# Kernel tuning notes

Measured on AMD Instinct MI355X. Metric: run time of the kernel, lower is better.

The kernel has to match this reference:

```python
import jax, jax.numpy as jnp
import numpy as np

M = 2048      # mention groups (spans with antecedents)
K_MAX = 128   # max antecedents per mention
N = 4096      # candidate span pool
G = 1000      # span representation dim
D = 20        # distance/genre/speaker embed dim
H = 150       # Score MLP hidden
GIJ = 3 * G + 3 * D  # 3060


def setup_inputs() -> dict:
    key = jax.random.key(0)
    ks = jax.random.split(key, 12)
    # ragged group lengths (deterministic): cycle 1..K_MAX, sum = P = 132096
    lengths = np.tile(np.arange(1, K_MAX + 1), M // K_MAX).astype(np.int32)
    P = int(lengths.sum())
    seg_ids = np.repeat(np.arange(M), lengths).astype(np.int32)
    starts = np.cumsum(lengths) - lengths
    offsets = (np.arange(P) - starts[seg_ids]).astype(np.int32)

    genre_emb = jax.random.normal(ks[3], (8, D), jnp.float32) * 0.02
    genre_emb = genre_emb.at[0].set(0.0)   # padding_idx=0
    speaker_emb = jax.random.normal(ks[4], (3, D), jnp.float32) * 0.02
    speaker_emb = speaker_emb.at[0].set(0.0)  # padding_idx=0

    return {
        "g_i": jax.random.normal(ks[0], (N, G), jnp.float32),
        "mention_scores": jax.random.normal(ks[1], (N, 1), jnp.float32),
        "dist_emb": jax.random.normal(ks[2], (9, D), jnp.float32) * 0.02,
        "genre_emb": genre_emb,
        "speaker_emb": speaker_emb,
        "W1": jax.random.normal(ks[5], (GIJ, H), jnp.float32) / np.sqrt(GIJ),
        "b1": jnp.zeros((H,), jnp.float32),
        "W2": jax.random.normal(ks[6], (H, H), jnp.float32) / np.sqrt(H),
        "b2": jnp.zeros((H,), jnp.float32),
        "W3": jax.random.normal(ks[7], (H, 1), jnp.float32) / np.sqrt(H),
        "b3": jnp.zeros((1,), jnp.float32),
        "mention_ids": jax.random.randint(ks[8], (P,), 0, N, jnp.int32),
        "antecedent_ids": jax.random.randint(ks[9], (P,), 0, N, jnp.int32),
        "dist_ids": jax.random.randint(ks[10], (P,), 0, 9, jnp.int32),
        "genre_ids": jax.random.randint(ks[11], (P,), 0, 8, jnp.int32),
        "speaker_ids": jax.random.randint(jax.random.fold_in(key, 99), (P,), 0, 3, jnp.int32),
        "lengths": jnp.asarray(lengths),
        "seg_ids": jnp.asarray(seg_ids),
        "offsets": jnp.asarray(offsets),
    }


def reference(g_i, mention_scores, dist_emb, genre_emb, speaker_emb,
              W1, b1, W2, b2, W3, b3,
              mention_ids, antecedent_ids, dist_ids, genre_ids, speaker_ids,
              lengths, seg_ids, offsets):
    # feature gathers: phi = [distance, genre, speaker] embeddings, (P, 3D)
    phi = jnp.concatenate(
        [dist_emb[dist_ids], genre_emb[genre_ids], speaker_emb[speaker_ids]], axis=1)
    i_g = g_i[mention_ids]      # (P, G)
    j_g = g_i[antecedent_ids]   # (P, G)
    pairs = jnp.concatenate([i_g, j_g, i_g * j_g, phi], axis=1)  # (P, GIJ)

    # 3-layer scoring MLP (dropout inactive at eval)
    h = jax.nn.relu(pairs @ W1 + b1)
    h = jax.nn.relu(h @ W2 + b2)
    s_ij = (h @ W3 + b3)[:, 0]  # (P,)

    scores = mention_scores[mention_ids, 0] + mention_scores[antecedent_ids, 0] + s_ij

    # per-group softmax over [group scores, epsilon=0] via segment ops
    seg_max = jax.ops.segment_max(scores, seg_ids, num_segments=M)
    m = jnp.maximum(seg_max, 0.0)                      # include epsilon 0
    e = jnp.exp(scores - m[seg_ids])                   # (P,)
    eps_e = jnp.exp(-m)                                # (M,)
    denom = jax.ops.segment_sum(e, seg_ids, num_segments=M) + eps_e
    pair_probs = e / denom[seg_ids]                    # (P,)
    eps_probs = eps_e / denom                          # (M,)

    # pad_and_stack(value=1000): row 0 is the empty leading group -> [1, 1000...]
    grid = jnp.full((M + 1, K_MAX + 1), 1000.0, dtype=scores.dtype)
    grid = grid.at[seg_ids + 1, offsets].set(pair_probs)
    grid = grid.at[jnp.arange(M) + 1, lengths].set(eps_probs)
    grid = grid.at[0, 0].set(1.0)
    return grid
```

## Files before the change

kernel.cpp:

```cpp
#include <hip/hip_runtime.h>

#define P_TOTAL 132096
#define NPOOL   4096
#define GDIM    1000
#define HDIM    150
#define MGRP    2048
#define KMAX    128

typedef __attribute__((ext_vector_type(4))) float f32x4;
typedef __attribute__((ext_vector_type(2))) float f32x2;
typedef __attribute__((ext_vector_type(4))) unsigned int u32x4;

#define OFF_W1C8   0
#define OFF_W1AB8  163840
#define OFF_W2F8   491520
#define OFF_ABPRE  517120
#define OFF_TABS2  3138560
#define OFF_SGRID  3276800
#define OFF_GF8    4325376
#define OFF_ITAB   8519680

__device__ __forceinline__ short f2bf(float f) {
  union { float f; unsigned u; } v; v.f = f;
  unsigned r = v.u + 0x7FFFu + ((v.u >> 16) & 1u);
  return (short)(r >> 16);
}
__device__ __forceinline__ float bf2f(unsigned short s) {
  return __builtin_bit_cast(float, ((unsigned)s) << 16);
}
__device__ __forceinline__ unsigned char f2fp8(float f) {
  int d = __builtin_amdgcn_cvt_pk_fp8_f32(f, 0.f, 0, false);
  return (unsigned char)(d & 0xFF);
}
__device__ __forceinline__ long mk64(unsigned lo, unsigned hi) {
  return (long)(((unsigned long long)hi << 32) | lo);
}

__device__ __forceinline__ u32x4 fp8prod16(u32x4 m, u32x4 a) {
  u32x4 r;
  #pragma unroll
  for (int d = 0; d < 4; ++d) {
    f32x2 ml = __builtin_amdgcn_cvt_pk_f32_fp8(m[d], false);
    f32x2 mh = __builtin_amdgcn_cvt_pk_f32_fp8(m[d], true);
    f32x2 al = __builtin_amdgcn_cvt_pk_f32_fp8(a[d], false);
    f32x2 ah = __builtin_amdgcn_cvt_pk_f32_fp8(a[d], true);
    f32x2 pl = ml * al, ph = mh * ah;
    int o = __builtin_amdgcn_cvt_pk_fp8_f32(pl[0], pl[1], 0, false);
    o = __builtin_amdgcn_cvt_pk_fp8_f32(ph[0], ph[1], o, true);
    r[d] = (unsigned)o;
  }
  return r;
}

__device__ __forceinline__ unsigned pk_bf16(float lo, float hi) {
  unsigned o;
  asm("v_cvt_pk_bf16_f32 %0, %1, %2" : "=v"(o) : "v"(lo), "v"(hi));
  return o;
}

#define S1 5120
#define S2 10240
#define S3 800
#define S4 (NPOOL*256)
#define S5 (216*160)
#define S6 P_TOTAL
__global__ __launch_bounds__(256) void prep_kernel(
    const float* __restrict__ W1, const float* __restrict__ W2,
    const float* __restrict__ g_i,
    const float* __restrict__ dist_emb, const float* __restrict__ genre_emb,
    const float* __restrict__ spk_emb, const float* __restrict__ b1,
    const int* __restrict__ did, const int* __restrict__ gid,
    const int* __restrict__ sid,
    unsigned char* __restrict__ w1c8, unsigned char* __restrict__ w1ab8,
    unsigned char* __restrict__ w2f8, unsigned* __restrict__ gf8,
    float* __restrict__ tabs2, unsigned char* __restrict__ itab8) {
  int idx = blockIdx.x * 256 + threadIdx.x;
  if (idx < S1) {
    int c = idx / 160, n = idx % 160;
    int s = c >> 1, j = c & 1;
    unsigned dw[8];
    #pragma unroll
    for (int d = 0; d < 8; ++d) {
      unsigned acc = 0;
      #pragma unroll
      for (int b = 0; b < 4; ++b) {
        int kk = d*4 + b;
        int g = kk >> 3, i = kk & 7;
        int q = g ^ ((n >> 2) & 3);
        int k = s*64 + q*16 + j*8 + i;
        float v = (k < GDIM && n < HDIM) ? W1[(2000 + k)*HDIM + n] : 0.f;
        acc |= ((unsigned)f2fp8(v)) << (8*b);
      }
      dw[d] = acc;
    }
    u32x4 lo = {dw[0], dw[1], dw[2], dw[3]};
    u32x4 hi = {dw[4], dw[5], dw[6], dw[7]};
    *(u32x4*)(w1c8 + c*5120 + n*32)      = lo;
    *(u32x4*)(w1c8 + c*5120 + n*32 + 16) = hi;
  } else if (idx < S1 + S2) {
    int i2 = idx - S1;
    int c = i2 / 320, n = i2 % 320;
    int s = c >> 2, j = c & 3;
    unsigned dw[8];
    #pragma unroll
    for (int d = 0; d < 8; ++d) {
      unsigned acc = 0;
      #pragma unroll
      for (int b = 0; b < 4; ++b) {
        int kk = d*4 + b;
        int g = kk >> 3, i = kk & 7;
        int k = s*128 + g*32 + j*8 + i;
        float v = 0.f;
        if (k < GDIM) {
          if (n < HDIM)                 v = W1[k*HDIM + n];
          else if (n >= 160 && n < 310) v = W1[(1000 + k)*HDIM + (n - 160)];
        }
        acc |= ((unsigned)f2fp8(v)) << (8*b);
      }
      dw[d] = acc;
    }
    u32x4 lo = {dw[0], dw[1], dw[2], dw[3]};
    u32x4 hi = {dw[4], dw[5], dw[6], dw[7]};
    *(u32x4*)(w1ab8 + c*10240 + n*32)      = lo;
    *(u32x4*)(w1ab8 + c*10240 + n*32 + 16) = hi;
  } else if (idx < S1 + S2 + S3) {
    int i2 = idx - S1 - S2;
    int c = i2 / 160, n = i2 % 160;
    unsigned dw[8];
    #pragma unroll
    for (int d = 0; d < 8; ++d) {
      unsigned acc = 0;
      #pragma unroll
      for (int b = 0; b < 4; ++b) {
        int kk = d*4 + b;
        int g = kk >> 3, ii = kk & 7;
        int q = g ^ ((n >> 2) & 3);
        int k = c*32 + q*8 + ii;
        float v = (k < HDIM && n < HDIM) ? W2[k*HDIM + n] : 0.f;
        acc |= ((unsigned)f2fp8(v)) << (8*b);
      }
      dw[d] = acc;
    }
    u32x4 lo = {dw[0], dw[1], dw[2], dw[3]};
    u32x4 hi = {dw[4], dw[5], dw[6], dw[7]};
    *(u32x4*)(w2f8 + c*5120 + n*32)      = lo;
    *(u32x4*)(w2f8 + c*5120 + n*32 + 16) = hi;
  } else if (idx < S1 + S2 + S3 + S4) {
    int i = idx - S1 - S2 - S3;
    int row = i >> 8, jd = i & 255;
    int c0 = jd * 4;
    float f0 = (c0     < GDIM) ? g_i[row*GDIM + c0]     : 0.f;
    float f1 = (c0 + 1 < GDIM) ? g_i[row*GDIM + c0 + 1] : 0.f;
    float f2 = (c0 + 2 < GDIM) ? g_i[row*GDIM + c0 + 2] : 0.f;
    float f3 = (c0 + 3 < GDIM) ? g_i[row*GDIM + c0 + 3] : 0.f;
    int d = 0;
    d = __builtin_amdgcn_cvt_pk_fp8_f32(f0, f1, d, false);
    d = __builtin_amdgcn_cvt_pk_fp8_f32(f2, f3, d, true);
    gf8[i] = (unsigned)d;
  } else if (idx < S1 + S2 + S3 + S4 + S5) {
    int i = idx - S1 - S2 - S3 - S4;
    int row = i / 160, n = i % 160;
    float acc = 0.f;
    if (n < HDIM) {
      int d = row / 24, g = (row / 3) % 8, sp = row % 3;
      acc = b1[n];
      #pragma unroll
      for (int kk = 0; kk < 20; ++kk) {
        acc += dist_emb [d*20 + kk]  * W1[(3000 + kk)*HDIM + n];
        acc += genre_emb[g*20 + kk]  * W1[(3020 + kk)*HDIM + n];
        acc += spk_emb  [sp*20 + kk] * W1[(3040 + kk)*HDIM + n];
      }
    }
    tabs2[i] = acc;
  } else if (idx < S1 + S2 + S3 + S4 + S5 + S6) {
    int p = idx - (S1 + S2 + S3 + S4 + S5);
    itab8[p] = (unsigned char)(did[p]*24 + gid[p]*3 + sid[p]);
  }
}

__global__ __launch_bounds__(256) void pre_gemm_kernel(
    const unsigned char* __restrict__ gf8, const unsigned char* __restrict__ w1ab8,
    unsigned short* __restrict__ abpre) {
  int wave = threadIdx.x >> 6, lane = threadIdx.x & 63;
  int quad = lane >> 4, n16 = lane & 15;
  int row0 = blockIdx.x * 64 + wave * 16;
  int col0 = blockIdx.y * 16;

  f32x4 acc = (f32x4){0.f, 0.f, 0.f, 0.f};
  const unsigned char* arow  = gf8 + (long)(row0 + n16) * 1024 + quad*32;
  const unsigned char* bbase = w1ab8 + ((long)col0 + n16) * 32 + quad*8;

  #pragma unroll 4
  for (int c = 0; c < 32; ++c) {
    long a = *(const long*)(arow + (c >> 2)*128 + (c & 3)*8);
    long b = *(const long*)(bbase + (long)c * 10240);
    acc = __builtin_amdgcn_mfma_f32_16x16x32_fp8_fp8(a, b, acc, 0, 0, 0);
  }
  #pragma unroll
  for (int r = 0; r < 4; ++r)
    abpre[(long)(row0 + quad*4 + r) * 320 + col0 + n16] = (unsigned short)f2bf(acc[r]);
}

__global__ __launch_bounds__(256) void mlp_kernel(
    const unsigned char* __restrict__ gf8,
    const unsigned* __restrict__ abpre32,
    const float* __restrict__ tabs2,
    const unsigned char* __restrict__ itab8,
    const unsigned char* __restrict__ w1c8,
    const unsigned char* __restrict__ w2f8,
    const float* __restrict__ ms,
    const float* __restrict__ W3, const float* __restrict__ b2,
    const float* __restrict__ b3,
    const int* __restrict__ mention_ids, const int* __restrict__ antecedent_ids,
    const int* __restrict__ seg_ids, const int* __restrict__ offs,
    float* __restrict__ sgrid) {

  __shared__ __align__(16) unsigned char lds[53248];

  int tid = threadIdx.x;
  int wave = tid >> 6, lane = tid & 63;
  int quad = lane >> 4, n16 = lane & 15;
  int lp0 = blockIdx.x * 128;
  int gp0 = lp0;
  int wrow = wave * 32;

  int jj = (lane & 3) ^ ((lane >> 2) & 3) ^ ((lane >> 4) & 1);
  int srow = lane >> 2;
  int swA = quad ^ (n16 & 3) ^ ((n16 >> 2) & 1);
  int swB = quad ^ ((n16 >> 2) & 3);

  const unsigned char* pA0 =
      gf8 + (long)mention_ids[gp0 + wave*16 + srow] * 1024 + jj*16;
  const unsigned char* pA1 =
      gf8 + (long)mention_ids[gp0 + (wave + 4)*16 + srow] * 1024 + jj*16;
  const unsigned char* pA2 =
      gf8 + (long)antecedent_ids[gp0 + wave*16 + srow] * 1024 + jj*16;
  const unsigned char* pA3 =
      gf8 + (long)antecedent_ids[gp0 + (wave + 4)*16 + srow] * 1024 + jj*16;
  int dA0 = wave*1024,      dA1 = (wave + 4)*1024;
  int dA2 = 8192 + dA0,     dA3 = 8192 + dA1;

  f32x4 acc0[10], acc1[10];
  #pragma unroll
  for (int t = 0; t < 10; ++t) {
    acc0[t] = (f32x4){0.f, 0.f, 0.f, 0.f};
    acc1[t] = (f32x4){0.f, 0.f, 0.f, 0.f};
  }

  auto issue = [&](int s, int buf) {
    unsigned char* base = lds + buf*26624;
    long so = (long)s * 64;
    __builtin_amdgcn_global_load_lds((const unsigned int*)(pA0 + so),
        (unsigned int*)(base + dA0 + lane*16), 16, 0, 0);
    __builtin_amdgcn_global_load_lds((const unsigned int*)(pA1 + so),
        (unsigned int*)(base + dA1 + lane*16), 16, 0, 0);
    __builtin_amdgcn_global_load_lds((const unsigned int*)(pA2 + so),
        (unsigned int*)(base + dA2 + lane*16), 16, 0, 0);
    __builtin_amdgcn_global_load_lds((const unsigned int*)(pA3 + so),
        (unsigned int*)(base + dA3 + lane*16), 16, 0, 0);
    const unsigned char* wsrc = w1c8 + (long)s*10240;
    __builtin_amdgcn_global_load_lds((const unsigned int*)(wsrc + wave*1024 + (long)lane*16),
        (unsigned int*)(base + 16384 + wave*1024 + lane*16), 16, 0, 0);
    __builtin_amdgcn_global_load_lds((const unsigned int*)(wsrc + (wave+4)*1024 + (long)lane*16),
        (unsigned int*)(base + 16384 + (wave+4)*1024 + lane*16), 16, 0, 0);
    if (wave < 2)
      __builtin_amdgcn_global_load_lds((const unsigned int*)(wsrc + (wave+8)*1024 + (long)lane*16),
          (unsigned int*)(base + 16384 + (wave+8)*1024 + lane*16), 16, 0, 0);
  };

  issue(0, 0);
  for (int s = 0; s < 16; ++s) {
    __syncthreads();
    if (s < 15) issue(s + 1, (s + 1) & 1);
    const unsigned char* cb = lds + (s & 1)*26624;

    u32x4 M0 = *(const u32x4*)(cb + (wrow + n16)*64 + swA*16);
    u32x4 C0 = *(const u32x4*)(cb + 8192 + (wrow + n16)*64 + swA*16);
    u32x4 M1 = *(const u32x4*)(cb + (wrow + 16 + n16)*64 + swA*16);
    u32x4 C1 = *(const u32x4*)(cb + 8192 + (wrow + 16 + n16)*64 + swA*16);
    u32x4 P0 = fp8prod16(M0, C0);
    u32x4 P1 = fp8prod16(M1, C1);

    #pragma unroll
    for (int j = 0; j < 2; ++j) {
      long a0 = (j == 0) ? mk64(P0[0], P0[1]) : mk64(P0[2], P0[3]);
      long a1 = (j == 0) ? mk64(P1[0], P1[1]) : mk64(P1[2], P1[3]);
      const unsigned char* bp = cb + 16384 + j*5120 + n16*32 + swB*8;
      #pragma unroll
      for (int t = 0; t < 10; ++t) {
        long b = *(const long*)(bp + t*512);
        acc0[t] = __builtin_amdgcn_mfma_f32_16x16x32_fp8_fp8(a0, b, acc0[t], 0, 0, 0);
        acc1[t] = __builtin_amdgcn_mfma_f32_16x16x32_fp8_fp8(a1, b, acc1[t], 0, 0, 0);
      }
    }
  }
  __syncthreads();

  unsigned* extw = (unsigned*)(lds + 23552 + wave*5376);
  const unsigned short* ext16 = (const unsigned short*)extw;
  unsigned char* h1w = lds + wave * 5888;
  int rowi = lane >> 2, q4 = lane & 3;

  #pragma unroll
  for (int p = 0; p < 2; ++p) {
    int gpe = gp0 + wrow + p*16 + rowi;
    int m  = mention_ids[gpe];
    int a  = antecedent_ids[gpe];
    int it = itab8[gpe];
    const u32x4* pm = (const u32x4*)(abpre32 + (long)m*160 + q4*20);
    const u32x4* pa = (const u32x4*)(abpre32 + (long)a*160 + 80 + q4*20);
    const f32x4* tb = (const f32x4*)(tabs2 + (long)it*160 + q4*40);
    #pragma unroll
    for (int k = 0; k < 5; ++k) {
      u32x4 um = pm[k], ua = pa[k];
      f32x4 ta = tb[2*k], tc = tb[2*k + 1];
      u32x4 ov;
      #pragma unroll
      for (int d = 0; d < 4; ++d) {
        float f0 = (d == 0) ? ta[0] : (d == 1) ? ta[2] : (d == 2) ? tc[0] : tc[2];
        float f1 = (d == 0) ? ta[1] : (d == 1) ? ta[3] : (d == 2) ? tc[1] : tc[3];
        float v0 = bf2f((unsigned short)(um[d] & 0xffff))
                 + bf2f((unsigned short)(ua[d] & 0xffff)) + f0;
        float v1 = bf2f((unsigned short)(um[d] >> 16))
                 + bf2f((unsigned short)(ua[d] >> 16)) + f1;
        ov[d] = pk_bf16(v0, v1);
      }
      *(u32x4*)(extw + rowi*84 + q4*20 + 4*k) = ov;
    }
    #pragma unroll
    for (int r = 0; r < 4; ++r) {
      int lr = quad*4 + r;
      #pragma unroll
      for (int t = 0; t < 10; ++t) {
        int n = t*16 + n16;
        float e = bf2f(ext16[lr*168 + n]);
        float v = ((p == 0) ? acc0[t][r] : acc1[t][r]) + e;
        h1w[(p*16 + lr)*184 + n] = f2fp8(fmaxf(v, 0.f));
      }
    }
    __syncthreads();
  }

  for (int r = wave; r < 25; r += 4) {
    __builtin_amdgcn_global_load_lds(
        (const unsigned int*)(w2f8 + r*1024 + (long)lane*16),
        (unsigned int*)(lds + 23552 + r*1024), 16, 0, 0);
  }

  float bias3 = b3[0];
  float w3v[10], b2v[10];
  #pragma unroll
  for (int t = 0; t < 10; ++t) {
    int n = t*16 + n16;
    w3v[t] = (n < HDIM) ? W3[n] : 0.f;
    b2v[t] = (n < HDIM) ? b2[n] : 0.f;
  }
  __syncthreads();

  #pragma unroll
  for (int tile = 0; tile < 2; ++tile) {
    f32x4 acc2[10];
    #pragma unroll
    for (int t = 0; t < 10; ++t) acc2[t] = (f32x4){0.f, 0.f, 0.f, 0.f};

    #pragma unroll
    for (int c = 0; c < 5; ++c) {
      long a = *(const long*)(h1w + (tile*16 + n16)*184 + c*32 + quad*8);
      const unsigned char* bp = lds + 23552 + (c*160 + n16)*32 + swB*8;
      #pragma unroll
      for (int t = 0; t < 10; ++t) {
        long b = *(const long*)(bp + t*512);
        acc2[t] = __builtin_amdgcn_mfma_f32_16x16x32_fp8_fp8(a, b, acc2[t], 0, 0, 0);
      }
    }

    float part[4] = {0.f, 0.f, 0.f, 0.f};
    #pragma unroll
    for (int t = 0; t < 10; ++t) {
      #pragma unroll
      for (int r = 0; r < 4; ++r) {
        float h2 = fmaxf(acc2[t][r] + b2v[t], 0.f);
        part[r] += h2 * w3v[t];
      }
    }
    for (int msk = 1; msk < 16; msk <<= 1) {
      #pragma unroll
      for (int r = 0; r < 4; ++r) part[r] += __shfl_xor(part[r], msk);
    }

    if (n16 == 0) {
      #pragma unroll
      for (int r = 0; r < 4; ++r) {
        int gp = gp0 + wrow + tile*16 + quad*4 + r;
        float sc = part[r] + bias3 + ms[mention_ids[gp]] + ms[antecedent_ids[gp]];
        sgrid[seg_ids[gp] * KMAX + offs[gp]] = sc;
      }
    }
  }
}

__global__ __launch_bounds__(128) void softmax_kernel(const float* __restrict__ sgrid,
                                                      const int* __restrict__ lengths,
                                                      float* __restrict__ out) {
  int b = blockIdx.x, t = threadIdx.x;
  if (b == 0) {
    out[t] = (t == 0) ? 1.0f : 1000.0f;
    if (t == 0) out[128] = 1000.0f;
    return;
  }
  int m = b - 1;
  int len = lengths[m];
  float s = (t < len) ? sgrid[m * KMAX + t] : -1e30f;

  __shared__ float redA[2];
  __shared__ float redB[2];

  float v = s;
  #pragma unroll
  for (int o = 32; o >= 1; o >>= 1) v = fmaxf(v, __shfl_xor(v, o));
  if ((t & 63) == 0) redA[t >> 6] = v;
  __syncthreads();
  float mx = fmaxf(fmaxf(redA[0], redA[1]), 0.0f);

  float e = (t < len) ? expf(s - mx) : 0.f;
  float sum = e;
  #pragma unroll
  for (int o = 32; o >= 1; o >>= 1) sum += __shfl_xor(sum, o);
  if ((t & 63) == 0) redB[t >> 6] = sum;
  __syncthreads();

  float eps_e = expf(-mx);
  float denom = redB[0] + redB[1] + eps_e;

  float* row = out + (long)(m + 1) * 129;
  float val;
  if (t < len)       val = e / denom;
  else if (t == len) val = eps_e / denom;
  else               val = 1000.0f;
  row[t] = val;
  if (t == 0) row[128] = (len == KMAX) ? (eps_e / denom) : 1000.0f;
}

extern "C" void kernel_launch(void* const* d_in, const int* in_sizes, int n_in,
                              void* d_out, int out_size, void* d_ws, size_t ws_size,
                              hipStream_t stream) {
  const float* g_i        = (const float*)d_in[0];
  const float* ms         = (const float*)d_in[1];
  const float* dist_emb   = (const float*)d_in[2];
  const float* genre_emb  = (const float*)d_in[3];
  const float* spk_emb    = (const float*)d_in[4];
  const float* W1         = (const float*)d_in[5];
  const float* b1         = (const float*)d_in[6];
  const float* W2         = (const float*)d_in[7];
  const float* b2         = (const float*)d_in[8];
  const float* W3         = (const float*)d_in[9];
  const float* b3         = (const float*)d_in[10];
  const int* mention_ids    = (const int*)d_in[11];
  const int* antecedent_ids = (const int*)d_in[12];
  const int* dist_ids       = (const int*)d_in[13];
  const int* genre_ids      = (const int*)d_in[14];
  const int* spk_ids        = (const int*)d_in[15];
  const int* lengths        = (const int*)d_in[16];
  const int* seg_ids        = (const int*)d_in[17];
  const int* offsets        = (const int*)d_in[18];

  char* ws = (char*)d_ws;
  unsigned char* w1c8  = (unsigned char*)(ws + OFF_W1C8);
  unsigned char* w1ab8 = (unsigned char*)(ws + OFF_W1AB8);
  unsigned char* w2f8  = (unsigned char*)(ws + OFF_W2F8);
  unsigned short* abpre = (unsigned short*)(ws + OFF_ABPRE);
  float* tabs2  = (float*)(ws + OFF_TABS2);
  float* sgrid  = (float*)(ws + OFF_SGRID);
  unsigned char* gf8  = (unsigned char*)(ws + OFF_GF8);
  unsigned char* itab8 = (unsigned char*)(ws + OFF_ITAB);

  const int prepN = S1 + S2 + S3 + S4 + S5 + S6;
  prep_kernel<<<(prepN + 255)/256, 256, 0, stream>>>(W1, W2, g_i,
                                                     dist_emb, genre_emb, spk_emb, b1,
                                                     dist_ids, genre_ids, spk_ids,
                                                     w1c8, w1ab8, w2f8,
                                                     (unsigned*)gf8, tabs2, itab8);
  dim3 gpre(NPOOL/64, 20);
  pre_gemm_kernel<<<gpre, 256, 0, stream>>>(gf8, w1ab8, abpre);
  mlp_kernel<<<P_TOTAL/128, 256, 0, stream>>>(gf8, (const unsigned*)abpre, tabs2, itab8,
                                              w1c8, w2f8, ms,
                                              W3, b2, b3,
                                              mention_ids, antecedent_ids,
                                              seg_ids, offsets, sgrid);
  softmax_kernel<<<MGRP + 1, 128, 0, stream>>>(sgrid, lengths, (float*)d_out);
}
```

Before: 214.2 us.

## Read MLP weights directly from global memory to shrink LDS and raise occupancy

The main MLP kernel no longer stages W1 and W2 tiles in shared memory. Each wave reads those weight fragments straight from global memory, which lets the LDS footprint drop from 52KB to 40KB and adds a launch-bounds hint for four blocks per CU. The h1 buffer gets an XOR swizzle in place of padding, and one barrier plus the W2 staging step are removed. The pre-GEMM kernel is restructured so each wave computes five 16-column tiles and reuses its A fragments across them. The risk is that direct global weight loads are less coalesced and rely on cache hits, which could expose latency in the MFMA loop.

```diff
diff --git a/kernel.cpp b/kernel.cpp
--- a/kernel.cpp
+++ b/kernel.cpp
@@ -178,30 +178,46 @@
   }
 }
 
-__global__ __launch_bounds__(256) void pre_gemm_kernel(
+__global__ __launch_bounds__(128) void pre_gemm_kernel(
     const unsigned char* __restrict__ gf8, const unsigned char* __restrict__ w1ab8,
     unsigned short* __restrict__ abpre) {
   int wave = threadIdx.x >> 6, lane = threadIdx.x & 63;
   int quad = lane >> 4, n16 = lane & 15;
-  int row0 = blockIdx.x * 64 + wave * 16;
-  int col0 = blockIdx.y * 16;
-
-  f32x4 acc = (f32x4){0.f, 0.f, 0.f, 0.f};
-  const unsigned char* arow  = gf8 + (long)(row0 + n16) * 1024 + quad*32;
-  const unsigned char* bbase = w1ab8 + ((long)col0 + n16) * 32 + quad*8;
-
-  #pragma unroll 4
-  for (int c = 0; c < 32; ++c) {
-    long a = *(const long*)(arow + (c >> 2)*128 + (c & 3)*8);
-    long b = *(const long*)(bbase + (long)c * 10240);
-    acc = __builtin_amdgcn_mfma_f32_16x16x32_fp8_fp8(a, b, acc, 0, 0, 0);
-  }
-  #pragma unroll
-  for (int r = 0; r < 4; ++r)
-    abpre[(long)(row0 + quad*4 + r) * 320 + col0 + n16] = (unsigned short)f2bf(acc[r]);
-}
-
-__global__ __launch_bounds__(256) void mlp_kernel(
+  int rowbase = blockIdx.x * 32 + wave * 16;
+  int colbase = blockIdx.y * 80;
+
+  f32x4 acc[5];
+  #pragma unroll
+  for (int t = 0; t < 5; ++t) acc[t] = (f32x4){0.f, 0.f, 0.f, 0.f};
+
+  const unsigned char* arow = gf8 + (long)(rowbase + n16) * 1024 + quad*32;
+
+  for (int s = 0; s < 8; ++s) {
+    u32x4 Aa = *(const u32x4*)(arow + s*128);
+    u32x4 Ab = *(const u32x4*)(arow + s*128 + 16);
+    #pragma unroll
+    for (int j = 0; j < 4; ++j) {
+      long a = (j == 0) ? mk64(Aa[0], Aa[1]) : (j == 1) ? mk64(Aa[2], Aa[3])
+             : (j == 2) ? mk64(Ab[0], Ab[1]) : mk64(Ab[2], Ab[3]);
+      const unsigned char* bp = w1ab8 + (((s*4 + j)*320 + colbase + n16) * 32 + quad*8);
+      #pragma unroll
+      for (int t = 0; t < 5; ++t) {
+        long b = *(const long*)(bp + t*16*32);
+        acc[t] = __builtin_amdgcn_mfma_f32_16x16x32_fp8_fp8(a, b, acc[t], 0, 0, 0);
+      }
+    }
+  }
+  #pragma unroll
+  for (int t = 0; t < 5; ++t) {
+    #pragma unroll
+    for (int r = 0; r < 4; ++r) {
+      int row = rowbase + quad*4 + r;
+      abpre[(long)row * 320 + colbase + t*16 + n16] = (unsigned short)f2bf(acc[t][r]);
+    }
+  }
+}
+
+__global__ __launch_bounds__(256, 4) void mlp_kernel(
     const unsigned char* __restrict__ gf8,
     const unsigned* __restrict__ abpre32,
     const float* __restrict__ tabs2,
@@ -215,7 +231,7 @@
     const int* __restrict__ seg_ids, const int* __restrict__ offs,
     float* __restrict__ sgrid) {
 
-  __shared__ __align__(16) unsigned char lds[53248];
+  __shared__ __align__(16) unsigned char lds[40960];
 
   int tid = threadIdx.x;
   int wave = tid >> 6, lane = tid & 63;
@@ -248,7 +264,7 @@
   }
 
   auto issue = [&](int s, int buf) {
-    unsigned char* base = lds + buf*26624;
+    unsigned char* base = lds + buf*16384;
     long so = (long)s * 64;
     __builtin_amdgcn_global_load_lds((const unsigned int*)(pA0 + so),
         (unsigned int*)(base + dA0 + lane*16), 16, 0, 0);
@@ -258,21 +274,13 @@
         (unsigned int*)(base + dA2 + lane*16), 16, 0, 0);
     __builtin_amdgcn_global_load_lds((const unsigned int*)(pA3 + so),
         (unsigned int*)(base + dA3 + lane*16), 16, 0, 0);
-    const unsigned char* wsrc = w1c8 + (long)s*10240;
-    __builtin_amdgcn_global_load_lds((const unsigned int*)(wsrc + wave*1024 + (long)lane*16),
-        (unsigned int*)(base + 16384 + wave*1024 + lane*16), 16, 0, 0);
-    __builtin_amdgcn_global_load_lds((const unsigned int*)(wsrc + (wave+4)*1024 + (long)lane*16),
-        (unsigned int*)(base + 16384 + (wave+4)*1024 + lane*16), 16, 0, 0);
-    if (wave < 2)
-      __builtin_amdgcn_global_load_lds((const unsigned int*)(wsrc + (wave+8)*1024 + (long)lane*16),
-          (unsigned int*)(base + 16384 + (wave+8)*1024 + lane*16), 16, 0, 0);
   };
 
   issue(0, 0);
   for (int s = 0; s < 16; ++s) {
     __syncthreads();
     if (s < 15) issue(s + 1, (s + 1) & 1);
-    const unsigned char* cb = lds + (s & 1)*26624;
+    const unsigned char* cb = lds + (s & 1)*16384;
 
     u32x4 M0 = *(const u32x4*)(cb + (wrow + n16)*64 + swA*16);
     u32x4 C0 = *(const u32x4*)(cb + 8192 + (wrow + n16)*64 + swA*16);
@@ -281,11 +289,12 @@
     u32x4 P0 = fp8prod16(M0, C0);
     u32x4 P1 = fp8prod16(M1, C1);
 
+    const unsigned char* wbase = w1c8 + (long)s*10240;
     #pragma unroll
     for (int j = 0; j < 2; ++j) {
       long a0 = (j == 0) ? mk64(P0[0], P0[1]) : mk64(P0[2], P0[3]);
       long a1 = (j == 0) ? mk64(P1[0], P1[1]) : mk64(P1[2], P1[3]);
-      const unsigned char* bp = cb + 16384 + j*5120 + n16*32 + swB*8;
+      const unsigned char* bp = wbase + j*5120 + n16*32 + swB*8;
       #pragma unroll
       for (int t = 0; t < 10; ++t) {
         long b = *(const long*)(bp + t*512);
@@ -296,9 +305,9 @@
   }
   __syncthreads();
 
-  unsigned* extw = (unsigned*)(lds + 23552 + wave*5376);
+  unsigned char* h1w = lds + wave * 5120;
+  unsigned* extw = (unsigned*)(lds + 20480 + wave*5120);
   const unsigned short* ext16 = (const unsigned short*)extw;
-  unsigned char* h1w = lds + wave * 5888;
   int rowi = lane >> 2, q4 = lane & 3;
 
   #pragma unroll
@@ -325,26 +334,21 @@
                  + bf2f((unsigned short)(ua[d] >> 16)) + f1;
         ov[d] = pk_bf16(v0, v1);
       }
-      *(u32x4*)(extw + rowi*84 + q4*20 + 4*k) = ov;
+      *(u32x4*)(extw + rowi*80 + q4*20 + 4*k) = ov;
     }
     #pragma unroll
     for (int r = 0; r < 4; ++r) {
       int lr = quad*4 + r;
+      int row = p*16 + lr;
+      int xr = (lr & 12) << 1;
       #pragma unroll
       for (int t = 0; t < 10; ++t) {
         int n = t*16 + n16;
-        float e = bf2f(ext16[lr*168 + n]);
+        float e = bf2f(ext16[lr*160 + n]);
         float v = ((p == 0) ? acc0[t][r] : acc1[t][r]) + e;
-        h1w[(p*16 + lr)*184 + n] = f2fp8(fmaxf(v, 0.f));
-      }
-    }
-    __syncthreads();
-  }
-
-  for (int r = wave; r < 25; r += 4) {
-    __builtin_amdgcn_global_load_lds(
-        (const unsigned int*)(w2f8 + r*1024 + (long)lane*16),
-        (unsigned int*)(lds + 23552 + r*1024), 16, 0, 0);
+        h1w[row*160 + (n ^ xr)] = f2fp8(fmaxf(v, 0.f));
+      }
+    }
   }
 
   float bias3 = b3[0];
@@ -355,7 +359,6 @@
     w3v[t] = (n < HDIM) ? W3[n] : 0.f;
     b2v[t] = (n < HDIM) ? b2[n] : 0.f;
   }
-  __syncthreads();
 
   #pragma unroll
   for (int tile = 0; tile < 2; ++tile) {
@@ -363,10 +366,12 @@
     #pragma unroll
     for (int t = 0; t < 10; ++t) acc2[t] = (f32x4){0.f, 0.f, 0.f, 0.f};
 
+    int row = tile*16 + n16;
+    int xr = (row & 12) << 1;
     #pragma unroll
     for (int c = 0; c < 5; ++c) {
-      long a = *(const long*)(h1w + (tile*16 + n16)*184 + c*32 + quad*8);
-      const unsigned char* bp = lds + 23552 + (c*160 + n16)*32 + swB*8;
+      long a = *(const long*)(h1w + row*160 + ((c*32 + quad*8) ^ xr));
+      const unsigned char* bp = w2f8 + ((long)c*160 + n16)*32 + swB*8;
       #pragma unroll
       for (int t = 0; t < 10; ++t) {
         long b = *(const long*)(bp + t*512);
@@ -480,8 +485,8 @@
                                                      dist_ids, genre_ids, spk_ids,
                                                      w1c8, w1ab8, w2f8,
                                                      (unsigned*)gf8, tabs2, itab8);
-  dim3 gpre(NPOOL/64, 20);
-  pre_gemm_kernel<<<gpre, 256, 0, stream>>>(gf8, w1ab8, abpre);
+  dim3 gpre(NPOOL/32, 4);
+  pre_gemm_kernel<<<gpre, 128, 0, stream>>>(gf8, w1ab8, abpre);
   mlp_kernel<<<P_TOTAL/128, 256, 0, stream>>>(gf8, (const unsigned*)abpre, tabs2, itab8,
                                               w1c8, w2f8, ms,
                                               W3, b2, b3,
```

Result: slower. 352.2 us (+64.4%).
